# Kernel tuning notes

Measured on AMD Instinct MI355X. Metric: run time of the kernel, lower is better.

## Reference

```python
import jax, jax.numpy as jnp
import numpy as np

AUX_LOSS_WEIGHT = 0.01
TOP_K = 2


def setup_inputs() -> dict:
    key = jax.random.key(0)
    k0, k1, k2, k3, k4 = jax.random.split(key, 5)
    B, S, H, I, E = 4, 2048, 1024, 2816, 8
    scale = 0.02
    x = jax.random.normal(k0, (B, S, H), dtype=jnp.float32)
    Wr = jax.random.normal(k1, (H, E), dtype=jnp.float32) * scale   # router
    Wg = jax.random.normal(k2, (E, H, I), dtype=jnp.float32) * scale  # gate proj per expert
    Wu = jax.random.normal(k3, (E, H, I), dtype=jnp.float32) * scale  # up proj per expert
    Wd = jax.random.normal(k4, (E, I, H), dtype=jnp.float32) * scale  # down proj per expert
    return {"x": x, "Wr": Wr, "Wg": Wg, "Wu": Wu, "Wd": Wd}


def reference(x, Wr, Wg, Wu, Wd):
    B, S, H = x.shape
    E = Wr.shape[1]
    xf = x.reshape(-1, H)                      # [T, H]

    # Router: softmax -> top-k -> renormalize top-k weights
    logits = xf @ Wr                           # [T, E]
    probs = jax.nn.softmax(logits, axis=-1)
    vals, idx = jax.lax.top_k(probs, TOP_K)    # [T, K]
    vals = vals / (vals.sum(axis=-1, keepdims=True) + 1e-9)

    # Aux load-balancing loss (matches torch: mean prob * mean one-hot load)
    oh = jax.nn.one_hot(idx, E, dtype=xf.dtype)        # [T, K, E]
    expert_load = oh.sum(axis=1).mean(axis=0)          # [E]
    expert_prob = probs.mean(axis=0)                   # [E]
    router_loss = E * jnp.sum(expert_prob * expert_load) * AUX_LOSS_WEIGHT

    # Per-token combine weight for each expert: c[t,e] = sum_k vals[t,k] * (idx[t,k]==e)
    comb = jnp.einsum('tk,tke->te', vals, oh)          # [T, E]

    # Loop over the small fixed set of experts (dense SwiGLU, masked-weighted combine;
    # identical math to gather -> expert -> weighted index_add scatter)
    def expert_step(acc, ew):
        wg, wu, wd, ce = ew                            # [H,I], [H,I], [I,H], [T]
        h = jax.nn.silu(xf @ wg) * (xf @ wu)           # [T, I]
        return acc + (h @ wd) * ce[:, None], None

    out, _ = jax.lax.scan(expert_step, jnp.zeros_like(xf), (Wg, Wu, Wd, comb.T))
    return out.reshape(B, S, H), router_loss
```

## Files before the change

kernel.cpp:

```cpp
#include <hip/hip_runtime.h>
#include <stdint.h>

#define T_TOK 8192
#define HD    1024
#define ID    2816
#define NE    8
#define RCAP  17408

typedef __bf16 bf16x8 __attribute__((ext_vector_type(8)));
typedef float  f32x4  __attribute__((ext_vector_type(4)));

__device__ __forceinline__ unsigned short f2bf(float f) {
  union { float f; unsigned u; } v; v.f = f;
  unsigned r = v.u + 0x7FFFu + ((v.u >> 16) & 1u);
  return (unsigned short)(r >> 16);
}

__device__ __forceinline__ void gl16(const void* g, void* l) {
  __builtin_amdgcn_global_load_lds((__attribute__((address_space(1))) void*)g,
                                   (__attribute__((address_space(3))) void*)l,
                                   16, 0, 0);
}

__global__ void k_cvt_x(const float* __restrict__ x, unsigned short* __restrict__ xb) {
  const int i = blockIdx.x * blockDim.x + threadIdx.x;
  const float4 v = ((const float4*)x)[i];
  ushort4 o;
  o.x = f2bf(v.x); o.y = f2bf(v.y); o.z = f2bf(v.z); o.w = f2bf(v.w);
  ((ushort4*)xb)[i] = o;
}

__global__ void k_transpose(const float* __restrict__ Wg, const float* __restrict__ Wu,
                            const float* __restrict__ Wd,
                            unsigned short* __restrict__ Wgt, unsigned short* __restrict__ Wut,
                            unsigned short* __restrict__ Wdt) {
  const int m = blockIdx.y;
  const float* src; unsigned short* dst; int R, C;
  if (m < 8)       { src = Wg + (size_t)m * HD * ID;        dst = Wgt + (size_t)m * HD * ID;        R = HD; C = ID; }
  else if (m < 16) { src = Wu + (size_t)(m - 8) * HD * ID;  dst = Wut + (size_t)(m - 8) * HD * ID;  R = HD; C = ID; }
  else             { src = Wd + (size_t)(m - 16) * HD * ID; dst = Wdt + (size_t)(m - 16) * HD * ID; R = ID; C = HD; }
  const int tc = C / 64;
  const int tr = blockIdx.x / tc, tcc = blockIdx.x % tc;
  const int r0 = tr * 64, c0 = tcc * 64;
  __shared__ unsigned short tile[64][68];
  const int t = threadIdx.x;
#pragma unroll
  for (int k = 0; k < 4; ++k) {
    const int c = t + k * 256;
    const int row = c >> 4, c4 = c & 15;
    const float4 v = *(const float4*)(src + (size_t)(r0 + row) * C + c0 + c4 * 4);
    tile[row][c4 * 4 + 0] = f2bf(v.x);
    tile[row][c4 * 4 + 1] = f2bf(v.y);
    tile[row][c4 * 4 + 2] = f2bf(v.z);
    tile[row][c4 * 4 + 3] = f2bf(v.w);
  }
  __syncthreads();
  const int orow = t >> 2, seg = t & 3;
  __align__(16) unsigned short tmp[16];
#pragma unroll
  for (int j = 0; j < 16; ++j) tmp[j] = tile[seg * 16 + j][orow];
  unsigned short* dp = dst + (size_t)(c0 + orow) * R + r0 + seg * 16;
  ((uint4*)dp)[0] = ((const uint4*)tmp)[0];
  ((uint4*)dp)[1] = ((const uint4*)tmp)[1];
}

__global__ void k_router(const float* __restrict__ x, const float* __restrict__ Wr,
                         int* __restrict__ cnt, float* __restrict__ psum,
                         int* __restrict__ tok_e, float* __restrict__ tok_w) {
  __shared__ float bp[NE];
  __shared__ int bc[NE];
  const int tid = threadIdx.x;
  if (tid < NE) { bp[tid] = 0.f; bc[tid] = 0; }
  __syncthreads();
  const int lane = tid & 63, w = tid >> 6;
  for (int i = 0; i < 8; ++i) {
    const int t = blockIdx.x * 32 + w * 8 + i;
    float acc[NE] = {0.f, 0.f, 0.f, 0.f, 0.f, 0.f, 0.f, 0.f};
    for (int h = lane; h < HD; h += 64) {
      const float xv = x[(size_t)t * HD + h];
      const float4 w0 = *(const float4*)(Wr + h * 8);
      const float4 w1 = *(const float4*)(Wr + h * 8 + 4);
      acc[0] += xv * w0.x; acc[1] += xv * w0.y; acc[2] += xv * w0.z; acc[3] += xv * w0.w;
      acc[4] += xv * w1.x; acc[5] += xv * w1.y; acc[6] += xv * w1.z; acc[7] += xv * w1.w;
    }
#pragma unroll
    for (int e = 0; e < NE; ++e)
      for (int off = 32; off > 0; off >>= 1)
        acc[e] += __shfl_xor(acc[e], off, 64);
    if (lane == 0) {
      float mx = acc[0];
      for (int e = 1; e < NE; ++e) mx = fmaxf(mx, acc[e]);
      float p[NE], s = 0.f;
      for (int e = 0; e < NE; ++e) { p[e] = __expf(acc[e] - mx); s += p[e]; }
      const float inv = 1.f / s;
      for (int e = 0; e < NE; ++e) p[e] *= inv;
      int e0 = 0;
      for (int e = 1; e < NE; ++e) if (p[e] > p[e0]) e0 = e;
      int e1 = (e0 == 0) ? 1 : 0;
      for (int e = 0; e < NE; ++e) if (e != e0 && p[e] > p[e1]) e1 = e;
      const float v0 = p[e0], v1 = p[e1];
      const float invs = 1.f / (v0 + v1 + 1e-9f);
      tok_e[2 * t] = e0;          tok_e[2 * t + 1] = e1;
      tok_w[2 * t] = v0 * invs;   tok_w[2 * t + 1] = v1 * invs;
      atomicAdd(&bc[e0], 1); atomicAdd(&bc[e1], 1);
      for (int e = 0; e < NE; ++e) atomicAdd(&bp[e], p[e]);
    }
  }
  __syncthreads();
  if (tid < NE) { atomicAdd(&cnt[tid], bc[tid]); atomicAdd(&psum[tid], bp[tid]); }
}

__global__ void k_offsets(const int* __restrict__ cnt, const float* __restrict__ psum,
                          int* __restrict__ offp, int* __restrict__ pair_tok,
                          float* __restrict__ pair_w, float* __restrict__ loss_out) {
  __shared__ int soff[NE + 1], scnt[NE];
  if (threadIdx.x == 0) {
    int o = 0;
    for (int e = 0; e < NE; ++e) {
      soff[e] = o; scnt[e] = cnt[e];
      o += (scnt[e] + 127) & ~127;
    }
    soff[NE] = o;
    for (int e = 0; e <= NE; ++e) offp[e] = soff[e];
    float loss = 0.f;
    for (int e = 0; e < NE; ++e) loss += psum[e] * (float)scnt[e];
    loss *= (float)NE * 0.01f / ((float)T_TOK * (float)T_TOK);
    *loss_out = loss;
  }
  __syncthreads();
  for (int e = 0; e < NE; ++e) {
    const int base = soff[e] + scnt[e];
    const int n = soff[e + 1] - base;
    for (int j = threadIdx.x; j < n; j += blockDim.x) {
      pair_tok[base + j] = -1;
      pair_w[base + j] = 0.f;
    }
  }
}

__global__ void k_scatter(const int* __restrict__ tok_e, const float* __restrict__ tok_w,
                          const int* __restrict__ offp, int* __restrict__ cursor,
                          int* __restrict__ pair_tok, float* __restrict__ pair_w) {
  const int t = blockIdx.x * 256 + threadIdx.x;
#pragma unroll
  for (int k = 0; k < 2; ++k) {
    const int e = tok_e[2 * t + k];
    const int pos = atomicAdd(&cursor[e], 1);
    const int idx = offp[e] + pos;
    pair_tok[idx] = t;
    pair_w[idx] = tok_w[2 * t + k];
  }
}

__launch_bounds__(256, 2)
__global__ void k_stage1(const unsigned short* __restrict__ xb,
                         const unsigned short* __restrict__ Wgt,
                         const unsigned short* __restrict__ Wut,
                         const int* __restrict__ offp,
                         const int* __restrict__ pair_tok,
                         unsigned short* __restrict__ act) {
  __shared__ __align__(16) unsigned short lA[8192];
  __shared__ __align__(16) unsigned short lBg[8192];
  __shared__ __align__(16) unsigned short lBu[8192];
  __shared__ int toks[128];

  const int row0 = blockIdx.y * 128;
  if (row0 >= offp[8]) return;
  int e = 0;
  while (offp[e + 1] <= row0) ++e;
  const int i0 = blockIdx.x * 128;
  const int tid = threadIdx.x;
  if (tid < 128) {
    const int tk = pair_tok[row0 + tid];
    toks[tid] = tk < 0 ? 0 : tk;
  }
  __syncthreads();

  const int lane = tid & 63, w = tid >> 6;
  const unsigned short* gA[4];
  const unsigned short* gBg[4];
  const unsigned short* gBu[4];
  unsigned ldso[4];
  const unsigned short* wgtE = Wgt + (size_t)e * ID * HD;
  const unsigned short* wutE = Wut + (size_t)e * ID * HD;
#pragma unroll
  for (int j = 0; j < 4; ++j) {
    const int row = (w * 4 + j) * 8 + (lane >> 3);
    const int kb = (lane & 7) ^ (row & 7);
    gA[j]  = xb + (size_t)toks[row] * HD + kb * 8;
    gBg[j] = wgtE + (size_t)(i0 + row) * HD + kb * 8;
    gBu[j] = wutE + (size_t)(i0 + row) * HD + kb * 8;
    ldso[j] = (unsigned)(w * 4 + j) * 512u;
  }

  const f32x4 zero = {0.f, 0.f, 0.f, 0.f};
  f32x4 accg[4][4], accu[4][4];
#pragma unroll
  for (int a = 0; a < 4; ++a)
#pragma unroll
    for (int b = 0; b < 4; ++b) { accg[a][b] = zero; accu[a][b] = zero; }

  const int wm = (w & 1) * 64, wn = (w >> 1) * 64;
  const int colm = lane & 15, quad = lane >> 4;

  for (int kt = 0; kt < HD / 64; ++kt) {
    __syncthreads();
    const int ko = kt * 64;
#pragma unroll
    for (int j = 0; j < 4; ++j) {
      gl16(gA[j] + ko,  &lA[ldso[j]]);
      gl16(gBg[j] + ko, &lBg[ldso[j]]);
      gl16(gBu[j] + ko, &lBu[ldso[j]]);
    }
    __syncthreads();
#pragma unroll
    for (int kk = 0; kk < 2; ++kk) {
      const int kbl = kk * 4 + quad;
      bf16x8 af[4], bg[4], bu[4];
#pragma unroll
      for (int mf = 0; mf < 4; ++mf) {
        const int r = wm + mf * 16 + colm;
        af[mf] = *(const bf16x8*)&lA[r * 64 + ((kbl ^ (r & 7)) * 8)];
      }
#pragma unroll
      for (int nf = 0; nf < 4; ++nf) {
        const int r = wn + nf * 16 + colm;
        const int o = r * 64 + ((kbl ^ (r & 7)) * 8);
        bg[nf] = *(const bf16x8*)&lBg[o];
        bu[nf] = *(const bf16x8*)&lBu[o];
      }
#pragma unroll
      for (int mf = 0; mf < 4; ++mf)
#pragma unroll
        for (int nf = 0; nf < 4; ++nf) {
          accg[mf][nf] = __builtin_amdgcn_mfma_f32_16x16x32_bf16(af[mf], bg[nf], accg[mf][nf], 0, 0, 0);
          accu[mf][nf] = __builtin_amdgcn_mfma_f32_16x16x32_bf16(af[mf], bu[nf], accu[mf][nf], 0, 0, 0);
        }
    }
  }

#pragma unroll
  for (int mf = 0; mf < 4; ++mf) {
#pragma unroll
    for (int r = 0; r < 4; ++r) {
      const int orow = row0 + wm + mf * 16 + quad * 4 + r;
      unsigned short* arow = act + (size_t)orow * ID + i0 + wn + colm;
#pragma unroll
      for (int nf = 0; nf < 4; ++nf) {
        const float g = accg[mf][nf][r];
        const float u = accu[mf][nf][r];
        const float h = (g / (1.f + __expf(-g))) * u;
        arow[nf * 16] = f2bf(h);
      }
    }
  }
}

__launch_bounds__(256, 2)
__global__ void k_stage2(const unsigned short* __restrict__ act,
                         const unsigned short* __restrict__ Wdt,
                         const int* __restrict__ offp,
                         const int* __restrict__ pair_tok,
                         const float* __restrict__ pair_w,
                         float* __restrict__ out) {
  __shared__ __align__(16) unsigned short lA[8192];
  __shared__ __align__(16) unsigned short lB[8192];
  __shared__ int toks[128];
  __shared__ float wts[128];

  const int row0 = blockIdx.y * 128;
  if (row0 >= offp[8]) return;
  int e = 0;
  while (offp[e + 1] <= row0) ++e;
  const int h0 = blockIdx.x * 128;
  const int tid = threadIdx.x;
  if (tid < 128) {
    toks[tid] = pair_tok[row0 + tid];
    wts[tid] = pair_w[row0 + tid];
  }
  const int lane = tid & 63, w = tid >> 6;
  const unsigned short* gA[4];
  const unsigned short* gB[4];
  unsigned ldso[4];
  const unsigned short* wdE = Wdt + (size_t)e * HD * ID;
#pragma unroll
  for (int j = 0; j < 4; ++j) {
    const int row = (w * 4 + j) * 8 + (lane >> 3);
    const int kb = (lane & 7) ^ (row & 7);
    gA[j] = act + (size_t)(row0 + row) * ID + kb * 8;
    gB[j] = wdE + (size_t)(h0 + row) * ID + kb * 8;
    ldso[j] = (unsigned)(w * 4 + j) * 512u;
  }

  const f32x4 zero = {0.f, 0.f, 0.f, 0.f};
  f32x4 acc[4][4];
#pragma unroll
  for (int a = 0; a < 4; ++a)
#pragma unroll
    for (int b = 0; b < 4; ++b) acc[a][b] = zero;

  const int wm = (w & 1) * 64, wn = (w >> 1) * 64;
  const int colm = lane & 15, quad = lane >> 4;

  for (int kt = 0; kt < ID / 64; ++kt) {
    __syncthreads();
    const int ko = kt * 64;
#pragma unroll
    for (int j = 0; j < 4; ++j) {
      gl16(gA[j] + ko, &lA[ldso[j]]);
      gl16(gB[j] + ko, &lB[ldso[j]]);
    }
    __syncthreads();
#pragma unroll
    for (int kk = 0; kk < 2; ++kk) {
      const int kbl = kk * 4 + quad;
      bf16x8 af[4], bf_[4];
#pragma unroll
      for (int mf = 0; mf < 4; ++mf) {
        const int r = wm + mf * 16 + colm;
        af[mf] = *(const bf16x8*)&lA[r * 64 + ((kbl ^ (r & 7)) * 8)];
      }
#pragma unroll
      for (int nf = 0; nf < 4; ++nf) {
        const int r = wn + nf * 16 + colm;
        bf_[nf] = *(const bf16x8*)&lB[r * 64 + ((kbl ^ (r & 7)) * 8)];
      }
#pragma unroll
      for (int mf = 0; mf < 4; ++mf)
#pragma unroll
        for (int nf = 0; nf < 4; ++nf)
          acc[mf][nf] = __builtin_amdgcn_mfma_f32_16x16x32_bf16(af[mf], bf_[nf], acc[mf][nf], 0, 0, 0);
    }
  }

#pragma unroll
  for (int mf = 0; mf < 4; ++mf) {
#pragma unroll
    for (int r = 0; r < 4; ++r) {
      const int lrow = wm + mf * 16 + quad * 4 + r;
      const int t = toks[lrow];
      if (t < 0) continue;
      const float wt = wts[lrow];
      float* orow = out + (size_t)t * HD + h0 + wn + colm;
#pragma unroll
      for (int nf = 0; nf < 4; ++nf)
        atomicAdd(&orow[nf * 16], wt * acc[mf][nf][r]);
    }
  }
}

extern "C" void kernel_launch(void* const* d_in, const int* in_sizes, int n_in,
                              void* d_out, int out_size, void* d_ws, size_t ws_size,
                              hipStream_t stream) {
  const float* x  = (const float*)d_in[0];
  const float* Wr = (const float*)d_in[1];
  const float* Wg = (const float*)d_in[2];
  const float* Wu = (const float*)d_in[3];
  const float* Wd = (const float*)d_in[4];
  float* out = (float*)d_out;

  char* ws = (char*)d_ws;
  const size_t off_xb  = 256;
  const size_t sz_xb   = (size_t)T_TOK * HD * 2;
  const size_t sz_w    = (size_t)NE * HD * ID * 2;
  const size_t off_wgt = off_xb + sz_xb;
  const size_t off_wut = off_wgt + sz_w;
  const size_t off_wdt = off_wut + sz_w;
  const size_t off_act = off_wdt + sz_w;
  const size_t sz_act  = (size_t)RCAP * ID * 2;
  const size_t off_ptk = off_act + sz_act;
  const size_t off_pw  = off_ptk + (size_t)RCAP * 4;
  const size_t off_te  = off_pw + (size_t)RCAP * 4;
  const size_t off_tw  = off_te + (size_t)T_TOK * 2 * 4;
  const size_t need    = off_tw + (size_t)T_TOK * 2 * 4;
  if (ws_size < need) return;

  int*   cnt    = (int*)(ws + 0);
  float* psum   = (float*)(ws + 32);
  int*   cursor = (int*)(ws + 64);
  int*   offp   = (int*)(ws + 96);
  unsigned short* xb  = (unsigned short*)(ws + off_xb);
  unsigned short* Wgt = (unsigned short*)(ws + off_wgt);
  unsigned short* Wut = (unsigned short*)(ws + off_wut);
  unsigned short* Wdt = (unsigned short*)(ws + off_wdt);
  unsigned short* act = (unsigned short*)(ws + off_act);
  int*   pair_tok = (int*)(ws + off_ptk);
  float* pair_w   = (float*)(ws + off_pw);
  int*   tok_e    = (int*)(ws + off_te);
  float* tok_w    = (float*)(ws + off_tw);

  hipMemsetAsync(ws, 0, 256, stream);
  hipMemsetAsync(out, 0, (size_t)T_TOK * HD * sizeof(float), stream);

  k_cvt_x<<<(T_TOK * HD / 4) / 256, 256, 0, stream>>>(x, xb);
  k_transpose<<<dim3(704, 24), 256, 0, stream>>>(Wg, Wu, Wd, Wgt, Wut, Wdt);
  k_router<<<T_TOK / 32, 256, 0, stream>>>(x, Wr, cnt, psum, tok_e, tok_w);
  k_offsets<<<1, 256, 0, stream>>>(cnt, psum, offp, pair_tok, pair_w, out + (size_t)T_TOK * HD);
  k_scatter<<<T_TOK / 256, 256, 0, stream>>>(tok_e, tok_w, offp, cursor, pair_tok, pair_w);
  k_stage1<<<dim3(ID / 128, RCAP / 128), 256, 0, stream>>>(xb, Wgt, Wut, offp, pair_tok, act);
  k_stage2<<<dim3(HD / 128, RCAP / 128), 256, 0, stream>>>(act, Wdt, offp, pair_tok, pair_w, out);
}
```

Before: 857.3 us.

## Replace atomic scatter-add with contrib buffer plus gather combine; retune transpose and router

After: 837.0 us. -2.4%, faster.

```diff
diff --git a/kernel.cpp b/kernel.cpp
--- a/kernel.cpp
+++ b/kernel.cpp
@@ -42,23 +42,31 @@
   const int tc = C / 64;
   const int tr = blockIdx.x / tc, tcc = blockIdx.x % tc;
   const int r0 = tr * 64, c0 = tcc * 64;
-  __shared__ unsigned short tile[64][68];
+  __shared__ __align__(16) unsigned short tl[64 * 64];
   const int t = threadIdx.x;
-#pragma unroll
-  for (int k = 0; k < 4; ++k) {
-    const int c = t + k * 256;
-    const int row = c >> 4, c4 = c & 15;
-    const float4 v = *(const float4*)(src + (size_t)(r0 + row) * C + c0 + c4 * 4);
-    tile[row][c4 * 4 + 0] = f2bf(v.x);
-    tile[row][c4 * 4 + 1] = f2bf(v.y);
-    tile[row][c4 * 4 + 2] = f2bf(v.z);
-    tile[row][c4 * 4 + 3] = f2bf(v.w);
+  const int rb = t >> 4;
+  const int c4 = t & 15;
+  const float* sp = src + (size_t)(r0 + rb * 4) * C + c0 + c4 * 4;
+  float4 v[4];
+#pragma unroll
+  for (int i = 0; i < 4; ++i) v[i] = *(const float4*)(sp + (size_t)i * C);
+  const float* vf = (const float*)v;
+#pragma unroll
+  for (int q = 0; q < 4; ++q) {
+    const int c = c4 * 4 + q;
+    ushort4 o;
+    o.x = f2bf(vf[0 * 4 + q]); o.y = f2bf(vf[1 * 4 + q]);
+    o.z = f2bf(vf[2 * 4 + q]); o.w = f2bf(vf[3 * 4 + q]);
+    *(ushort4*)&tl[c * 64 + ((rb ^ (c & 15)) * 4)] = o;
   }
   __syncthreads();
   const int orow = t >> 2, seg = t & 3;
   __align__(16) unsigned short tmp[16];
 #pragma unroll
-  for (int j = 0; j < 16; ++j) tmp[j] = tile[seg * 16 + j][orow];
+  for (int mI = 0; mI < 4; ++mI) {
+    const int s = seg * 4 + mI;
+    *(ushort4*)&tmp[mI * 4] = *(const ushort4*)&tl[orow * 64 + ((s ^ (orow & 15)) * 4)];
+  }
   unsigned short* dp = dst + (size_t)(c0 + orow) * R + r0 + seg * 16;
   ((uint4*)dp)[0] = ((const uint4*)tmp)[0];
   ((uint4*)dp)[1] = ((const uint4*)tmp)[1];
@@ -73,38 +81,36 @@
   if (tid < NE) { bp[tid] = 0.f; bc[tid] = 0; }
   __syncthreads();
   const int lane = tid & 63, w = tid >> 6;
-  for (int i = 0; i < 8; ++i) {
-    const int t = blockIdx.x * 32 + w * 8 + i;
-    float acc[NE] = {0.f, 0.f, 0.f, 0.f, 0.f, 0.f, 0.f, 0.f};
-    for (int h = lane; h < HD; h += 64) {
-      const float xv = x[(size_t)t * HD + h];
-      const float4 w0 = *(const float4*)(Wr + h * 8);
-      const float4 w1 = *(const float4*)(Wr + h * 8 + 4);
-      acc[0] += xv * w0.x; acc[1] += xv * w0.y; acc[2] += xv * w0.z; acc[3] += xv * w0.w;
-      acc[4] += xv * w1.x; acc[5] += xv * w1.y; acc[6] += xv * w1.z; acc[7] += xv * w1.w;
-    }
-#pragma unroll
-    for (int e = 0; e < NE; ++e)
-      for (int off = 32; off > 0; off >>= 1)
-        acc[e] += __shfl_xor(acc[e], off, 64);
-    if (lane == 0) {
-      float mx = acc[0];
-      for (int e = 1; e < NE; ++e) mx = fmaxf(mx, acc[e]);
-      float p[NE], s = 0.f;
-      for (int e = 0; e < NE; ++e) { p[e] = __expf(acc[e] - mx); s += p[e]; }
-      const float inv = 1.f / s;
-      for (int e = 0; e < NE; ++e) p[e] *= inv;
-      int e0 = 0;
-      for (int e = 1; e < NE; ++e) if (p[e] > p[e0]) e0 = e;
-      int e1 = (e0 == 0) ? 1 : 0;
-      for (int e = 0; e < NE; ++e) if (e != e0 && p[e] > p[e1]) e1 = e;
-      const float v0 = p[e0], v1 = p[e1];
-      const float invs = 1.f / (v0 + v1 + 1e-9f);
-      tok_e[2 * t] = e0;          tok_e[2 * t + 1] = e1;
-      tok_w[2 * t] = v0 * invs;   tok_w[2 * t + 1] = v1 * invs;
-      atomicAdd(&bc[e0], 1); atomicAdd(&bc[e1], 1);
-      for (int e = 0; e < NE; ++e) atomicAdd(&bp[e], p[e]);
-    }
+  const int t = blockIdx.x * 4 + w;
+  float acc[NE] = {0.f, 0.f, 0.f, 0.f, 0.f, 0.f, 0.f, 0.f};
+  for (int h = lane; h < HD; h += 64) {
+    const float xv = x[(size_t)t * HD + h];
+    const float4 w0 = *(const float4*)(Wr + h * 8);
+    const float4 w1 = *(const float4*)(Wr + h * 8 + 4);
+    acc[0] += xv * w0.x; acc[1] += xv * w0.y; acc[2] += xv * w0.z; acc[3] += xv * w0.w;
+    acc[4] += xv * w1.x; acc[5] += xv * w1.y; acc[6] += xv * w1.z; acc[7] += xv * w1.w;
+  }
+#pragma unroll
+  for (int e = 0; e < NE; ++e)
+    for (int off = 32; off > 0; off >>= 1)
+      acc[e] += __shfl_xor(acc[e], off, 64);
+  if (lane == 0) {
+    float mx = acc[0];
+    for (int e = 1; e < NE; ++e) mx = fmaxf(mx, acc[e]);
+    float p[NE], s = 0.f;
+    for (int e = 0; e < NE; ++e) { p[e] = __expf(acc[e] - mx); s += p[e]; }
+    const float inv = 1.f / s;
+    for (int e = 0; e < NE; ++e) p[e] *= inv;
+    int e0 = 0;
+    for (int e = 1; e < NE; ++e) if (p[e] > p[e0]) e0 = e;
+    int e1 = (e0 == 0) ? 1 : 0;
+    for (int e = 0; e < NE; ++e) if (e != e0 && p[e] > p[e1]) e1 = e;
+    const float v0 = p[e0], v1 = p[e1];
+    const float invs = 1.f / (v0 + v1 + 1e-9f);
+    tok_e[2 * t] = e0;          tok_e[2 * t + 1] = e1;
+    tok_w[2 * t] = v0 * invs;   tok_w[2 * t + 1] = v1 * invs;
+    atomicAdd(&bc[e0], 1); atomicAdd(&bc[e1], 1);
+    for (int e = 0; e < NE; ++e) atomicAdd(&bp[e], p[e]);
   }
   __syncthreads();
   if (tid < NE) { atomicAdd(&cnt[tid], bc[tid]); atomicAdd(&psum[tid], bp[tid]); }
@@ -140,7 +146,8 @@
 
 __global__ void k_scatter(const int* __restrict__ tok_e, const float* __restrict__ tok_w,
                           const int* __restrict__ offp, int* __restrict__ cursor,
-                          int* __restrict__ pair_tok, float* __restrict__ pair_w) {
+                          int* __restrict__ pair_tok, float* __restrict__ pair_w,
+                          int* __restrict__ inv_p) {
   const int t = blockIdx.x * 256 + threadIdx.x;
 #pragma unroll
   for (int k = 0; k < 2; ++k) {
@@ -149,6 +156,7 @@
     const int idx = offp[e] + pos;
     pair_tok[idx] = t;
     pair_w[idx] = tok_w[2 * t + k];
+    inv_p[2 * t + k] = idx;
   }
 }
 
@@ -256,13 +264,15 @@
   }
 }
 
+template <bool USE_CONTRIB>
 __launch_bounds__(256, 2)
-__global__ void k_stage2(const unsigned short* __restrict__ act,
-                         const unsigned short* __restrict__ Wdt,
-                         const int* __restrict__ offp,
-                         const int* __restrict__ pair_tok,
-                         const float* __restrict__ pair_w,
-                         float* __restrict__ out) {
+__global__ void k_stage2_t(const unsigned short* __restrict__ act,
+                           const unsigned short* __restrict__ Wdt,
+                           const int* __restrict__ offp,
+                           const int* __restrict__ pair_tok,
+                           const float* __restrict__ pair_w,
+                           float* __restrict__ contrib,
+                           float* __restrict__ out) {
   __shared__ __align__(16) unsigned short lA[8192];
   __shared__ __align__(16) unsigned short lB[8192];
   __shared__ int toks[128];
@@ -274,7 +284,7 @@
   while (offp[e + 1] <= row0) ++e;
   const int h0 = blockIdx.x * 128;
   const int tid = threadIdx.x;
-  if (tid < 128) {
+  if (!USE_CONTRIB && tid < 128) {
     toks[tid] = pair_tok[row0 + tid];
     wts[tid] = pair_w[row0 + tid];
   }
@@ -338,15 +348,38 @@
 #pragma unroll
     for (int r = 0; r < 4; ++r) {
       const int lrow = wm + mf * 16 + quad * 4 + r;
-      const int t = toks[lrow];
-      if (t < 0) continue;
-      const float wt = wts[lrow];
-      float* orow = out + (size_t)t * HD + h0 + wn + colm;
-#pragma unroll
-      for (int nf = 0; nf < 4; ++nf)
-        atomicAdd(&orow[nf * 16], wt * acc[mf][nf][r]);
-    }
-  }
+      if (USE_CONTRIB) {
+        float* crow = contrib + (size_t)(row0 + lrow) * HD + h0 + wn + colm;
+#pragma unroll
+        for (int nf = 0; nf < 4; ++nf)
+          crow[nf * 16] = acc[mf][nf][r];
+      } else {
+        const int t = toks[lrow];
+        if (t < 0) continue;
+        const float wt = wts[lrow];
+        float* orow = out + (size_t)t * HD + h0 + wn + colm;
+#pragma unroll
+        for (int nf = 0; nf < 4; ++nf)
+          atomicAdd(&orow[nf * 16], wt * acc[mf][nf][r]);
+      }
+    }
+  }
+}
+
+__global__ void k_combine(const float* __restrict__ contrib, const int* __restrict__ inv_p,
+                          const float* __restrict__ tok_w, float* __restrict__ out) {
+  const int t = blockIdx.x;
+  const int h4 = threadIdx.x;
+  const int p0 = inv_p[2 * t], p1 = inv_p[2 * t + 1];
+  const float w0 = tok_w[2 * t], w1 = tok_w[2 * t + 1];
+  const float4 a = ((const float4*)(contrib + (size_t)p0 * HD))[h4];
+  const float4 b = ((const float4*)(contrib + (size_t)p1 * HD))[h4];
+  float4 o;
+  o.x = w0 * a.x + w1 * b.x;
+  o.y = w0 * a.y + w1 * b.y;
+  o.z = w0 * a.z + w1 * b.z;
+  o.w = w0 * a.w + w1 * b.w;
+  ((float4*)(out + (size_t)t * HD))[h4] = o;
 }
 
 extern "C" void kernel_launch(void* const* d_in, const int* in_sizes, int n_in,
@@ -372,8 +405,12 @@
   const size_t off_pw  = off_ptk + (size_t)RCAP * 4;
   const size_t off_te  = off_pw + (size_t)RCAP * 4;
   const size_t off_tw  = off_te + (size_t)T_TOK * 2 * 4;
-  const size_t need    = off_tw + (size_t)T_TOK * 2 * 4;
-  if (ws_size < need) return;
+  const size_t off_ip  = off_tw + (size_t)T_TOK * 2 * 4;
+  const size_t off_ctb = off_ip + (size_t)T_TOK * 2 * 4;
+  const size_t need_base = off_ctb;
+  const size_t need_full = off_ctb + (size_t)RCAP * HD * 4;
+  if (ws_size < need_base) return;
+  const bool use_contrib = (ws_size >= need_full);
 
   int*   cnt    = (int*)(ws + 0);
   float* psum   = (float*)(ws + 32);
@@ -388,15 +425,23 @@
   float* pair_w   = (float*)(ws + off_pw);
   int*   tok_e    = (int*)(ws + off_te);
   float* tok_w    = (float*)(ws + off_tw);
+  int*   inv_p    = (int*)(ws + off_ip);
+  float* contrib  = (float*)(ws + off_ctb);
 
   hipMemsetAsync(ws, 0, 256, stream);
-  hipMemsetAsync(out, 0, (size_t)T_TOK * HD * sizeof(float), stream);
+  if (!use_contrib)
+    hipMemsetAsync(out, 0, (size_t)T_TOK * HD * sizeof(float), stream);
 
   k_cvt_x<<<(T_TOK * HD / 4) / 256, 256, 0, stream>>>(x, xb);
   k_transpose<<<dim3(704, 24), 256, 0, stream>>>(Wg, Wu, Wd, Wgt, Wut, Wdt);
-  k_router<<<T_TOK / 32, 256, 0, stream>>>(x, Wr, cnt, psum, tok_e, tok_w);
+  k_router<<<T_TOK / 4, 256, 0, stream>>>(x, Wr, cnt, psum, tok_e, tok_w);
   k_offsets<<<1, 256, 0, stream>>>(cnt, psum, offp, pair_tok, pair_w, out + (size_t)T_TOK * HD);
-  k_scatter<<<T_TOK / 256, 256, 0, stream>>>(tok_e, tok_w, offp, cursor, pair_tok, pair_w);
+  k_scatter<<<T_TOK / 256, 256, 0, stream>>>(tok_e, tok_w, offp, cursor, pair_tok, pair_w, inv_p);
   k_stage1<<<dim3(ID / 128, RCAP / 128), 256, 0, stream>>>(xb, Wgt, Wut, offp, pair_tok, act);
-  k_stage2<<<dim3(HD / 128, RCAP / 128), 256, 0, stream>>>(act, Wdt, offp, pair_tok, pair_w, out);
-}
+  if (use_contrib) {
+    k_stage2_t<true><<<dim3(HD / 128, RCAP / 128), 256, 0, stream>>>(act, Wdt, offp, pair_tok, pair_w, contrib, out);
+    k_combine<<<T_TOK, 256, 0, stream>>>(contrib, inv_p, tok_w, out);
+  } else {
+    k_stage2_t<false><<<dim3(HD / 128, RCAP / 128), 256, 0, stream>>>(act, Wdt, offp, pair_tok, pair_w, contrib, out);
+  }
+}
```
